# Kernel optimization log

Measured on AMD Instinct MI355X. Metric: run time of the kernel, lower is better.

The kernel has to match this reference:

```python
import jax, jax.numpy as jnp
import numpy as np

N, K, D, E, H, O = 8192, 16, 256, 128, 512, 256


def _mlp(v, W1, W2):
    # nn.Sequential(Linear(no bias), Tanh, Linear(no bias)) with torch [out,in] weights
    return jnp.tanh(v @ W1.T) @ W2.T


def setup_inputs() -> dict:
    key = jax.random.key(0)
    ks = jax.random.split(key, 16)
    def rn(k, shape, s=1.0):
        return jax.random.normal(k, shape, jnp.float32) * s
    return {
        "x": rn(ks[0], (N, D)),
        "neibs": rn(ks[1], (N * K, D)),
        "edge_emb": rn(ks[2], (N * K, E)),
        "mask": jax.random.randint(ks[3], (N, K), 0, 2, jnp.int32),
        "W1x": rn(ks[4], (H, D), 0.02), "W2x": rn(ks[5], (H, H), 0.02),
        "W1n": rn(ks[6], (H, D), 0.02), "W2n": rn(ks[7], (H, H), 0.02),
        "W1e": rn(ks[8], (H, E), 0.02), "W2e": rn(ks[9], (H, H), 0.02),
        "Wfx": rn(ks[10], (O, D), 0.02), "bfx": jnp.zeros((O,), jnp.float32),
        "Wfn": rn(ks[11], (O, D), 0.02), "bfn": jnp.zeros((O,), jnp.float32),
        "Wfe": rn(ks[12], (O, E), 0.02), "bfe": jnp.zeros((O,), jnp.float32),
    }


def reference(x, neibs, edge_emb, mask, W1x, W2x, W1n, W2n, W1e, W2e,
              Wfx, bfx, Wfn, bfn, Wfe, bfe):
    n, d = x.shape
    e = edge_emb.shape[1]
    x_att = _mlp(x, W1x, W2x)                                  # [N,H]
    neib_att = _mlp(neibs, W1n, W2n).reshape(n, -1, H)         # [N,K,H]
    edge_att = _mlp(edge_emb, W1e, W2e).reshape(n, -1, H)      # [N,K,H]

    # node-neighbor attention (scaled by hard-coded sqrt(512))
    ws = jnp.einsum('nkh,nh->nk', neib_att, x_att) / np.sqrt(512.0).astype(np.float32)
    ws = jax.nn.softmax(ws, axis=1)
    agg_neib = jnp.einsum('nk,nkd->nd', ws, neibs.reshape(n, -1, d))
    out = jnp.concatenate([x @ Wfx.T + bfx, agg_neib @ Wfn.T + bfn], axis=1)

    # node-edge attention (unscaled, masked)
    ws2 = jnp.einsum('nkh,nh->nk', edge_att, x_att)
    ws2 = ws2 + (-9999999.0) * mask.astype(x.dtype)
    ws2 = jax.nn.softmax(ws2, axis=1)
    agg_edge = jnp.einsum('nk,nke->ne', ws2, edge_emb.reshape(n, -1, e))
    out = jnp.concatenate([out, agg_edge @ Wfe.T + bfe], axis=1)  # [N,3*O]
    return jax.nn.relu(out)
```

## Files before the change

### kernel.cpp

```cpp
#include <hip/hip_runtime.h>
#include <hip/hip_bf16.h>

typedef __bf16 bf16;
typedef __bf16 bf16x2 __attribute__((ext_vector_type(2)));
typedef __bf16 bf16x4 __attribute__((ext_vector_type(4)));
typedef __bf16 bf16x8 __attribute__((ext_vector_type(8)));
typedef float  f32x4  __attribute__((ext_vector_type(4)));

__device__ __forceinline__ void async16(const bf16* g, bf16* l) {
  __builtin_amdgcn_global_load_lds(
      (__attribute__((address_space(1))) void*)g,
      (__attribute__((address_space(3))) void*)l,
      16, 0, 0);
}

template<int N>
__device__ __forceinline__ void vm_wait() {
  asm volatile("s_waitcnt vmcnt(%0)" :: "i"(N) : "memory");
}

__device__ __forceinline__ void hard_barrier() {
  asm volatile("" ::: "memory");
  __builtin_amdgcn_s_barrier();
  asm volatile("" ::: "memory");
}

__device__ __forceinline__ void fence_barrier() {
  asm volatile("s_waitcnt vmcnt(0) lgkmcnt(0)" ::: "memory");
  __syncthreads();
}

__device__ __forceinline__ float fast_tanh(float x) {
  float e = __builtin_amdgcn_exp2f(x * 2.88539008177793f);
  return 1.f - 2.f * __builtin_amdgcn_rcpf(e + 1.f);
}

__device__ __forceinline__ int swz(int elem, int row) {
  return elem ^ ((row & 7) << 3);
}

template<int ACT, typename OT>
__global__ __launch_bounds__(256, 4)
void gemm64(const bf16* __restrict__ A, const bf16* __restrict__ W,
            OT* __restrict__ C, int K, int ldc, float alpha,
            const float* __restrict__ bias) {
  __shared__ bf16 As[2][64 * 64];
  __shared__ bf16 Bs[2][64 * 64];
  const int tid  = threadIdx.x;
  const int wave = tid >> 6, lane = tid & 63;
  const int wr = wave >> 1, wc = wave & 1;
  const int g = lane >> 4, l4 = lane & 15;

  f32x4 acc[2][2];
#pragma unroll
  for (int i = 0; i < 2; ++i)
#pragma unroll
    for (int j = 0; j < 2; ++j)
      acc[i][j] = (f32x4){0.f, 0.f, 0.f, 0.f};

  const bf16* Abase = A + (size_t)blockIdx.x * 64 * K;
  const bf16* Wbase = W + (size_t)blockIdx.y * 64 * K;

  auto stage = [&](int buf, int k0) {
#pragma unroll
    for (int i = 0; i < 2; ++i) {
      const int cb  = i * 256 + wave * 64;
      const int c   = cb + lane;
      const int row = c >> 3;
      const int kk  = ((c & 7) ^ (row & 7)) << 3;
      async16(Abase + (size_t)row * K + k0 + kk, &As[buf][cb * 8]);
      async16(Wbase + (size_t)row * K + k0 + kk, &Bs[buf][cb * 8]);
    }
  };

  const int nt = K >> 6;
  stage(0, 0);
  for (int t = 0; t < nt; ++t) {
    const int buf = t & 1;
    if (t + 1 < nt) { stage(buf ^ 1, (t + 1) * 64); vm_wait<4>(); }
    else            { vm_wait<0>(); }
    hard_barrier();
#pragma unroll
    for (int s = 0; s < 2; ++s) {
      const int koff = s * 32 + g * 8;
      bf16x8 af[2], bfr[2];
#pragma unroll
      for (int i = 0; i < 2; ++i) {
        const int ra = wr * 32 + i * 16 + l4;
        af[i] = *(const bf16x8*)&As[buf][ra * 64 + swz(koff, ra)];
      }
#pragma unroll
      for (int j = 0; j < 2; ++j) {
        const int rb = wc * 32 + j * 16 + l4;
        bfr[j] = *(const bf16x8*)&Bs[buf][rb * 64 + swz(koff, rb)];
      }
#pragma unroll
      for (int i = 0; i < 2; ++i)
#pragma unroll
        for (int j = 0; j < 2; ++j)
          acc[i][j] = __builtin_amdgcn_mfma_f32_16x16x32_bf16(af[i], bfr[j], acc[i][j], 0, 0, 0);
    }
    hard_barrier();
  }

  const int rbase = blockIdx.x * 64 + wr * 32;
  const int cbase = blockIdx.y * 64 + wc * 32;
#pragma unroll
  for (int i = 0; i < 2; ++i)
#pragma unroll
    for (int j = 0; j < 2; ++j) {
      const int col = cbase + j * 16 + l4;
      const float bv = bias ? bias[col] : 0.f;
#pragma unroll
      for (int r = 0; r < 4; ++r) {
        const int row = rbase + i * 16 + g * 4 + r;
        float v = acc[i][j][r] * alpha + bv;
        if (ACT == 1) v = fast_tanh(v);
        if (ACT == 2) v = fmaxf(v, 0.f);
        C[(size_t)row * ldc + col] = (OT)v;
      }
    }
}

template<int D>
__global__ __launch_bounds__(256, 2)
void score_agg(const float* __restrict__ A, const bf16* __restrict__ Wb,
               const bf16* __restrict__ y, int ldy, int yoff, float scale,
               const int* __restrict__ mask, bf16* __restrict__ agg) {
  __shared__ bf16 As[64 * D];
  __shared__ bf16 Bs[2][256 * 32];
  float* sred = (float*)(&Bs[0][0]);
  float* wgt  = (float*)(&Bs[0][0]) + 256;
  const int tid  = threadIdx.x;
  const int wave = tid >> 6, lane = tid & 63;
  const int g = lane >> 4, l4 = lane & 15;
  const int blk = blockIdx.x;

  constexpr int NP = D / 32;
  constexpr int NS = 2 * NP;

  auto stageB = [&](int s, int buf) {
    const int j  = s / NP, ph = s % NP;
    const bf16* Wsrc = Wb + (size_t)j * 256 * D + ph * 32;
#pragma unroll
    for (int i = 0; i < 4; ++i) {
      const int cb  = i * 256 + wave * 64;
      const int c   = cb + lane;
      const int row = c >> 2;
      const int sl  = (c & 3) ^ ((row >> 1) & 3);
      async16(Wsrc + (size_t)row * D + sl * 8, &Bs[buf][cb * 8]);
    }
  };

  stageB(0, 0);

  const float* Ab = A + (size_t)blk * 64 * D;
  constexpr int F4PR = D / 4;
#pragma unroll
  for (int ii = 0; ii < D / 16; ++ii) {
    const int c    = ii * 256 + tid;
    const int row  = c / F4PR;
    const int col4 = (c % F4PR) * 4;
    const float4 v = *(const float4*)(Ab + (size_t)row * D + col4);
    bf16x4 o = {(bf16)v.x, (bf16)v.y, (bf16)v.z, (bf16)v.w};
    *(bf16x4*)&As[row * D + swz(col4, row)] = o;
  }

  float p[4][4];
#pragma unroll
  for (int i = 0; i < 4; ++i)
#pragma unroll
    for (int r = 0; r < 4; ++r) p[i][r] = 0.f;

  fence_barrier();

  int s = 0;
  for (int j = 0; j < 2; ++j) {
    f32x4 acc[4][4];
#pragma unroll
    for (int i = 0; i < 4; ++i)
#pragma unroll
      for (int jj = 0; jj < 4; ++jj)
        acc[i][jj] = (f32x4){0.f, 0.f, 0.f, 0.f};

#pragma unroll
    for (int ph = 0; ph < NP; ++ph) {
      const int buf = s & 1;
      if (s + 1 < NS) { stageB(s + 1, buf ^ 1); vm_wait<4>(); }
      else            { vm_wait<0>(); }
      hard_barrier();

      const int ka = ph * 32 + g * 8;
      bf16x8 af[4], bfr[4];
#pragma unroll
      for (int i = 0; i < 4; ++i) {
        const int ra = i * 16 + l4;
        af[i] = *(const bf16x8*)&As[ra * D + swz(ka, ra)];
      }
#pragma unroll
      for (int jj = 0; jj < 4; ++jj) {
        const int rb = wave * 64 + jj * 16 + l4;
        const int sl = g ^ ((rb >> 1) & 3);
        bfr[jj] = *(const bf16x8*)&Bs[buf][rb * 32 + sl * 8];
      }
#pragma unroll
      for (int i = 0; i < 4; ++i)
#pragma unroll
        for (int jj = 0; jj < 4; ++jj)
          acc[i][jj] = __builtin_amdgcn_mfma_f32_16x16x32_bf16(af[i], bfr[jj], acc[i][jj], 0, 0, 0);

      hard_barrier();
      ++s;
    }

#pragma unroll
    for (int i = 0; i < 4; ++i) {
      const size_t yb = (size_t)(blk * 4 + i) * ldy + yoff + j * 256 + wave * 64;
#pragma unroll
      for (int jj = 0; jj < 4; ++jj) {
        const float yv = (float)y[yb + jj * 16 + l4];
        p[i][0] += fast_tanh(acc[i][jj][0]) * yv;
        p[i][1] += fast_tanh(acc[i][jj][1]) * yv;
        p[i][2] += fast_tanh(acc[i][jj][2]) * yv;
        p[i][3] += fast_tanh(acc[i][jj][3]) * yv;
      }
    }
  }

#pragma unroll
  for (int i = 0; i < 4; ++i)
#pragma unroll
    for (int r = 0; r < 4; ++r) {
      float v = p[i][r];
#pragma unroll
      for (int m = 1; m < 16; m <<= 1) v += __shfl_xor(v, m);
      p[i][r] = v;
    }
  if (l4 == 0) {
#pragma unroll
    for (int i = 0; i < 4; ++i)
#pragma unroll
      for (int r = 0; r < 4; ++r)
        sred[wave * 64 + i * 16 + g * 4 + r] = p[i][r];
  }
  __syncthreads();

  if (tid < 64) {
    const int node_g = blk * 4 + (tid >> 4);
    float sv = (sred[tid] + sred[64 + tid] + sred[128 + tid] + sred[192 + tid]) * scale;
    if (mask) sv -= 9999999.0f * (float)mask[node_g * 16 + (tid & 15)];
    float m = sv;
#pragma unroll
    for (int d = 1; d < 16; d <<= 1) m = fmaxf(m, __shfl_xor(m, d));
    float e = __builtin_amdgcn_exp2f((sv - m) * 1.44269504088896f);
    float sum = e;
#pragma unroll
    for (int d = 1; d < 16; d <<= 1) sum += __shfl_xor(sum, d);
    wgt[tid] = e / sum;
  }
  __syncthreads();

  constexpr int EPT = D / 64;
  const int n  = tid >> 6;
  const int dl = (tid & 63) * EPT;
  float a[EPT];
#pragma unroll
  for (int e = 0; e < EPT; ++e) a[e] = 0.f;
#pragma unroll
  for (int k = 0; k < 16; ++k) {
    const float w = wgt[n * 16 + k];
    const int rk = n * 16 + k;
    if constexpr (EPT == 4) {
      bf16x4 v = *(const bf16x4*)&As[rk * D + swz(dl, rk)];
      a[0] += w * (float)v[0]; a[1] += w * (float)v[1];
      a[2] += w * (float)v[2]; a[3] += w * (float)v[3];
    } else {
      bf16x2 v = *(const bf16x2*)&As[rk * D + swz(dl, rk)];
      a[0] += w * (float)v[0]; a[1] += w * (float)v[1];
    }
  }
  if constexpr (EPT == 4) {
    bf16x4 o = {(bf16)a[0], (bf16)a[1], (bf16)a[2], (bf16)a[3]};
    *(bf16x4*)&agg[(size_t)(blk * 4 + n) * D + dl] = o;
  } else {
    bf16x2 o = {(bf16)a[0], (bf16)a[1]};
    *(bf16x2*)&agg[(size_t)(blk * 4 + n) * D + dl] = o;
  }
}

struct CvtEnt { const float* s; bf16* d; int n; };
struct CvtArgs { CvtEnt e[8]; };

__global__ void cvt_small(CvtArgs args) {
  const CvtEnt ent = args.e[blockIdx.y];
  const int i = blockIdx.x * 2048 + threadIdx.x * 8;
  if (i < ent.n) {
    const float4 a = *(const float4*)(ent.s + i);
    const float4 c = *(const float4*)(ent.s + i + 4);
    bf16x8 o = { (bf16)a.x, (bf16)a.y, (bf16)a.z, (bf16)a.w,
                 (bf16)c.x, (bf16)c.y, (bf16)c.z, (bf16)c.w };
    *(bf16x8*)(ent.d + i) = o;
  }
}

__global__ void transpose2(const float* __restrict__ s0, bf16* __restrict__ d0,
                           const float* __restrict__ s1, bf16* __restrict__ d1) {
  __shared__ float t[16][17];
  const float* s = blockIdx.z ? s1 : s0;
  bf16* d = blockIdx.z ? d1 : d0;
  const int x0 = blockIdx.x * 16, y0 = blockIdx.y * 16;
  t[threadIdx.y][threadIdx.x] = s[(size_t)(y0 + threadIdx.y) * 512 + x0 + threadIdx.x];
  __syncthreads();
  d[(size_t)(x0 + threadIdx.y) * 512 + (y0 + threadIdx.x)] = (bf16)t[threadIdx.x][threadIdx.y];
}

extern "C" void kernel_launch(void* const* d_in, const int* in_sizes, int n_in,
                              void* d_out, int out_size, void* d_ws, size_t ws_size,
                              hipStream_t stream) {
  const float* x     = (const float*)d_in[0];
  const float* neibs = (const float*)d_in[1];
  const float* edge  = (const float*)d_in[2];
  const int*   mask  = (const int*)d_in[3];
  const float* W1x = (const float*)d_in[4];
  const float* W2x = (const float*)d_in[5];
  const float* W1n = (const float*)d_in[6];
  const float* W2n = (const float*)d_in[7];
  const float* W1e = (const float*)d_in[8];
  const float* W2e = (const float*)d_in[9];
  const float* Wfx = (const float*)d_in[10];
  const float* bfx = (const float*)d_in[11];
  const float* Wfn = (const float*)d_in[12];
  const float* bfn = (const float*)d_in[13];
  const float* Wfe = (const float*)d_in[14];
  const float* bfe = (const float*)d_in[15];
  float* out = (float*)d_out;

  char* wsb = (char*)d_ws;
  const size_t MB = 1024 * 1024;
  bf16* W2nT = (bf16*)(wsb + 0);
  bf16* W2eT = (bf16*)(wsb + 512 * 1024);
  char* wtb  = wsb + 1 * MB;
  bf16* W1xb = (bf16*)(wtb + 0);
  bf16* W2xb = (bf16*)(wtb + 256 * 1024);
  bf16* W1nb = (bf16*)(wtb + 768 * 1024);
  bf16* W1eb = (bf16*)(wtb + 1024 * 1024);
  bf16* Wfxb = (bf16*)(wtb + 1152 * 1024);
  bf16* Wfnb = (bf16*)(wtb + 1280 * 1024);
  bf16* Wfeb = (bf16*)(wtb + 1408 * 1024);
  bf16* xb    = (bf16*)(wsb + 3 * MB);
  bf16* h_x   = (bf16*)(wsb + 7 * MB);
  bf16* x_att = (bf16*)(wsb + 15 * MB);
  bf16* ycat  = (bf16*)(wsb + 23 * MB);
  bf16* aggn  = (bf16*)(wsb + 39 * MB);
  bf16* agge  = (bf16*)(wsb + 43 * MB);

  const float inv_sqrt512 = 0.04419417382415922f;

  CvtArgs ca;
  ca.e[0] = {x,   xb,   2097152};
  ca.e[1] = {W1x, W1xb, 131072};
  ca.e[2] = {W2x, W2xb, 262144};
  ca.e[3] = {W1n, W1nb, 131072};
  ca.e[4] = {W1e, W1eb, 65536};
  ca.e[5] = {Wfx, Wfxb, 65536};
  ca.e[6] = {Wfn, Wfnb, 65536};
  ca.e[7] = {Wfe, Wfeb, 32768};
  cvt_small<<<dim3(1024, 8), 256, 0, stream>>>(ca);

  transpose2<<<dim3(32, 32, 2), dim3(16, 16), 0, stream>>>(W2n, W2nT, W2e, W2eT);

  gemm64<1, bf16><<<dim3(128, 8), 256, 0, stream>>>(xb, W1xb, h_x, 256, 512, 1.f, nullptr);
  gemm64<0, bf16><<<dim3(128, 8), 256, 0, stream>>>(h_x, W2xb, x_att, 512, 512, 1.f, nullptr);
  gemm64<0, bf16><<<dim3(128, 16), 256, 0, stream>>>(x_att, W2nT, ycat, 512, 1024, 1.f, nullptr);

  score_agg<256><<<2048, 256, 0, stream>>>(neibs, W1nb, ycat, 1024, 0, inv_sqrt512, nullptr, aggn);
  score_agg<128><<<2048, 256, 0, stream>>>(edge,  W1eb, ycat, 1024, 512, 1.f, mask, agge);

  gemm64<2, float><<<dim3(128, 4), 256, 0, stream>>>(xb,   Wfxb, out + 0,   256, 768, 1.f, bfx);
  gemm64<2, float><<<dim3(128, 4), 256, 0, stream>>>(aggn, Wfnb, out + 256, 256, 768, 1.f, bfn);
  gemm64<2, float><<<dim3(128, 4), 256, 0, stream>>>(agge, Wfeb, out + 512, 128, 768, 1.f, bfe);
}
```

Baseline: 395.5 us.

## Merge prologue and tail launches, hoist y loads, add MFMA priority hints

Folds the weight conversion and both transposes into one prologue kernel, and the three final projection GEMMs into one 3-way batched launch. The aim is fewer kernel launches and better use of the GPU for small grids. score_agg now preloads the y values into registers before the main loop instead of reading them in the epilogue. s_setprio is set around the MFMA clusters in both GEMM kernels. The hoisted y values raise register pressure in score_agg, and the transpose blocks now run serially inside the prologue.

```diff
diff --git a/kernel.cpp b/kernel.cpp
--- a/kernel.cpp
+++ b/kernel.cpp
@@ -40,12 +40,11 @@
 }
 
 template<int ACT, typename OT>
-__global__ __launch_bounds__(256, 4)
-void gemm64(const bf16* __restrict__ A, const bf16* __restrict__ W,
-            OT* __restrict__ C, int K, int ldc, float alpha,
-            const float* __restrict__ bias) {
-  __shared__ bf16 As[2][64 * 64];
-  __shared__ bf16 Bs[2][64 * 64];
+__device__ __forceinline__
+void gemm64_body(const bf16* __restrict__ A, const bf16* __restrict__ W,
+                 OT* __restrict__ C, int K, int ldc, float alpha,
+                 const float* __restrict__ bias,
+                 int bx, int by, bf16* As , bf16* Bs ) {
   const int tid  = threadIdx.x;
   const int wave = tid >> 6, lane = tid & 63;
   const int wr = wave >> 1, wc = wave & 1;
@@ -58,8 +57,8 @@
     for (int j = 0; j < 2; ++j)
       acc[i][j] = (f32x4){0.f, 0.f, 0.f, 0.f};
 
-  const bf16* Abase = A + (size_t)blockIdx.x * 64 * K;
-  const bf16* Wbase = W + (size_t)blockIdx.y * 64 * K;
+  const bf16* Abase = A + (size_t)bx * 64 * K;
+  const bf16* Wbase = W + (size_t)by * 64 * K;
 
   auto stage = [&](int buf, int k0) {
 #pragma unroll
@@ -68,8 +67,8 @@
       const int c   = cb + lane;
       const int row = c >> 3;
       const int kk  = ((c & 7) ^ (row & 7)) << 3;
-      async16(Abase + (size_t)row * K + k0 + kk, &As[buf][cb * 8]);
-      async16(Wbase + (size_t)row * K + k0 + kk, &Bs[buf][cb * 8]);
+      async16(Abase + (size_t)row * K + k0 + kk, &As[buf * 4096 + cb * 8]);
+      async16(Wbase + (size_t)row * K + k0 + kk, &Bs[buf * 4096 + cb * 8]);
     }
   };
 
@@ -87,24 +86,26 @@
 #pragma unroll
       for (int i = 0; i < 2; ++i) {
         const int ra = wr * 32 + i * 16 + l4;
-        af[i] = *(const bf16x8*)&As[buf][ra * 64 + swz(koff, ra)];
+        af[i] = *(const bf16x8*)&As[buf * 4096 + ra * 64 + swz(koff, ra)];
       }
 #pragma unroll
       for (int j = 0; j < 2; ++j) {
         const int rb = wc * 32 + j * 16 + l4;
-        bfr[j] = *(const bf16x8*)&Bs[buf][rb * 64 + swz(koff, rb)];
-      }
+        bfr[j] = *(const bf16x8*)&Bs[buf * 4096 + rb * 64 + swz(koff, rb)];
+      }
+      __builtin_amdgcn_s_setprio(1);
 #pragma unroll
       for (int i = 0; i < 2; ++i)
 #pragma unroll
         for (int j = 0; j < 2; ++j)
           acc[i][j] = __builtin_amdgcn_mfma_f32_16x16x32_bf16(af[i], bfr[j], acc[i][j], 0, 0, 0);
+      __builtin_amdgcn_s_setprio(0);
     }
     hard_barrier();
   }
 
-  const int rbase = blockIdx.x * 64 + wr * 32;
-  const int cbase = blockIdx.y * 64 + wc * 32;
+  const int rbase = bx * 64 + wr * 32;
+  const int cbase = by * 64 + wc * 32;
 #pragma unroll
   for (int i = 0; i < 2; ++i)
 #pragma unroll
@@ -120,6 +121,28 @@
         C[(size_t)row * ldc + col] = (OT)v;
       }
     }
+}
+
+template<int ACT, typename OT>
+__global__ __launch_bounds__(256, 4)
+void gemm64(const bf16* __restrict__ A, const bf16* __restrict__ W,
+            OT* __restrict__ C, int K, int ldc, float alpha,
+            const float* __restrict__ bias) {
+  __shared__ bf16 As[2 * 64 * 64];
+  __shared__ bf16 Bs[2 * 64 * 64];
+  gemm64_body<ACT, OT>(A, W, C, K, ldc, alpha, bias, blockIdx.x, blockIdx.y, As, Bs);
+}
+
+struct TailEnt { const bf16* A; const bf16* W; const float* bias; int K; int coff; };
+struct TailArgs { TailEnt e[3]; };
+
+__global__ __launch_bounds__(256, 4)
+void gemm64_tail(TailArgs args, float* __restrict__ out) {
+  __shared__ bf16 As[2 * 64 * 64];
+  __shared__ bf16 Bs[2 * 64 * 64];
+  const TailEnt ent = args.e[blockIdx.z];
+  gemm64_body<2, float>(ent.A, ent.W, out + ent.coff, ent.K, 768, 1.f, ent.bias,
+                        blockIdx.x, blockIdx.y, As, Bs);
 }
 
 template<int D>
@@ -154,6 +177,17 @@
 
   stageB(0, 0);
 
+  float yv[2][4][4];
+#pragma unroll
+  for (int j = 0; j < 2; ++j)
+#pragma unroll
+    for (int i = 0; i < 4; ++i) {
+      const size_t yb = (size_t)(blk * 4 + i) * ldy + yoff + j * 256 + wave * 64;
+#pragma unroll
+      for (int jj = 0; jj < 4; ++jj)
+        yv[j][i][jj] = (float)y[yb + jj * 16 + l4];
+    }
+
   const float* Ab = A + (size_t)blk * 64 * D;
   constexpr int F4PR = D / 4;
 #pragma unroll
@@ -203,11 +237,13 @@
         const int sl = g ^ ((rb >> 1) & 3);
         bfr[jj] = *(const bf16x8*)&Bs[buf][rb * 32 + sl * 8];
       }
+      __builtin_amdgcn_s_setprio(1);
 #pragma unroll
       for (int i = 0; i < 4; ++i)
 #pragma unroll
         for (int jj = 0; jj < 4; ++jj)
           acc[i][jj] = __builtin_amdgcn_mfma_f32_16x16x32_bf16(af[i], bfr[jj], acc[i][jj], 0, 0, 0);
+      __builtin_amdgcn_s_setprio(0);
 
       hard_barrier();
       ++s;
@@ -215,14 +251,13 @@
 
 #pragma unroll
     for (int i = 0; i < 4; ++i) {
-      const size_t yb = (size_t)(blk * 4 + i) * ldy + yoff + j * 256 + wave * 64;
 #pragma unroll
       for (int jj = 0; jj < 4; ++jj) {
-        const float yv = (float)y[yb + jj * 16 + l4];
-        p[i][0] += fast_tanh(acc[i][jj][0]) * yv;
-        p[i][1] += fast_tanh(acc[i][jj][1]) * yv;
-        p[i][2] += fast_tanh(acc[i][jj][2]) * yv;
-        p[i][3] += fast_tanh(acc[i][jj][3]) * yv;
+        const float yvv = yv[j][i][jj];
+        p[i][0] += fast_tanh(acc[i][jj][0]) * yvv;
+        p[i][1] += fast_tanh(acc[i][jj][1]) * yvv;
+        p[i][2] += fast_tanh(acc[i][jj][2]) * yvv;
+        p[i][3] += fast_tanh(acc[i][jj][3]) * yvv;
       }
     }
   }
@@ -289,29 +324,37 @@
 }
 
 struct CvtEnt { const float* s; bf16* d; int n; };
-struct CvtArgs { CvtEnt e[8]; };
-
-__global__ void cvt_small(CvtArgs args) {
-  const CvtEnt ent = args.e[blockIdx.y];
-  const int i = blockIdx.x * 2048 + threadIdx.x * 8;
-  if (i < ent.n) {
-    const float4 a = *(const float4*)(ent.s + i);
-    const float4 c = *(const float4*)(ent.s + i + 4);
-    bf16x8 o = { (bf16)a.x, (bf16)a.y, (bf16)a.z, (bf16)a.w,
-                 (bf16)c.x, (bf16)c.y, (bf16)c.z, (bf16)c.w };
-    *(bf16x8*)(ent.d + i) = o;
-  }
-}
-
-__global__ void transpose2(const float* __restrict__ s0, bf16* __restrict__ d0,
-                           const float* __restrict__ s1, bf16* __restrict__ d1) {
-  __shared__ float t[16][17];
-  const float* s = blockIdx.z ? s1 : s0;
-  bf16* d = blockIdx.z ? d1 : d0;
-  const int x0 = blockIdx.x * 16, y0 = blockIdx.y * 16;
-  t[threadIdx.y][threadIdx.x] = s[(size_t)(y0 + threadIdx.y) * 512 + x0 + threadIdx.x];
-  __syncthreads();
-  d[(size_t)(x0 + threadIdx.y) * 512 + (y0 + threadIdx.x)] = (bf16)t[threadIdx.x][threadIdx.y];
+struct CvtArgs {
+  CvtEnt e[8];
+  const float* t0s; bf16* t0d;
+  const float* t1s; bf16* t1d;
+};
+
+__global__ void prologue(CvtArgs args) {
+  if (blockIdx.y < 8) {
+    const CvtEnt ent = args.e[blockIdx.y];
+    const int i = blockIdx.x * 2048 + threadIdx.x * 8;
+    if (i < ent.n) {
+      const float4 a = *(const float4*)(ent.s + i);
+      const float4 c = *(const float4*)(ent.s + i + 4);
+      bf16x8 o = { (bf16)a.x, (bf16)a.y, (bf16)a.z, (bf16)a.w,
+                   (bf16)c.x, (bf16)c.y, (bf16)c.z, (bf16)c.w };
+      *(bf16x8*)(ent.d + i) = o;
+    }
+  } else {
+    __shared__ float t[16][17];
+    const int tx = threadIdx.x & 15, ty = threadIdx.x >> 4;
+    const int x0 = (blockIdx.x & 31) * 16, y0 = (blockIdx.x >> 5) * 16;
+#pragma unroll
+    for (int z = 0; z < 2; ++z) {
+      const float* s = z ? args.t1s : args.t0s;
+      bf16* d = z ? args.t1d : args.t0d;
+      t[ty][tx] = s[(size_t)(y0 + ty) * 512 + x0 + tx];
+      __syncthreads();
+      d[(size_t)(x0 + ty) * 512 + (y0 + tx)] = (bf16)t[tx][ty];
+      __syncthreads();
+    }
+  }
 }
 
 extern "C" void kernel_launch(void* const* d_in, const int* in_sizes, int n_in,
@@ -365,9 +408,9 @@
   ca.e[5] = {Wfx, Wfxb, 65536};
   ca.e[6] = {Wfn, Wfnb, 65536};
   ca.e[7] = {Wfe, Wfeb, 32768};
-  cvt_small<<<dim3(1024, 8), 256, 0, stream>>>(ca);
-
-  transpose2<<<dim3(32, 32, 2), dim3(16, 16), 0, stream>>>(W2n, W2nT, W2e, W2eT);
+  ca.t0s = W2n; ca.t0d = W2nT;
+  ca.t1s = W2e; ca.t1d = W2eT;
+  prologue<<<dim3(1024, 9), 256, 0, stream>>>(ca);
 
   gemm64<1, bf16><<<dim3(128, 8), 256, 0, stream>>>(xb, W1xb, h_x, 256, 512, 1.f, nullptr);
   gemm64<0, bf16><<<dim3(128, 8), 256, 0, stream>>>(h_x, W2xb, x_att, 512, 512, 1.f, nullptr);
@@ -376,7 +419,9 @@
   score_agg<256><<<2048, 256, 0, stream>>>(neibs, W1nb, ycat, 1024, 0, inv_sqrt512, nullptr, aggn);
   score_agg<128><<<2048, 256, 0, stream>>>(edge,  W1eb, ycat, 1024, 512, 1.f, mask, agge);
 
-  gemm64<2, float><<<dim3(128, 4), 256, 0, stream>>>(xb,   Wfxb, out + 0,   256, 768, 1.f, bfx);
-  gemm64<2, float><<<dim3(128, 4), 256, 0, stream>>>(aggn, Wfnb, out + 256, 256, 768, 1.f, bfn);
-  gemm64<2, float><<<dim3(128, 4), 256, 0, stream>>>(agge, Wfeb, out + 512, 128, 768, 1.f, bfe);
-}
+  TailArgs ta;
+  ta.e[0] = {xb,   Wfxb, bfx, 256, 0};
+  ta.e[1] = {aggn, Wfnb, bfn, 256, 256};
+  ta.e[2] = {agge, Wfeb, bfe, 128, 512};
+  gemm64_tail<<<dim3(128, 4, 3), 256, 0, stream>>>(ta, out);
+}
```

Result: faster. 385.6 us (-2.5%).
